# Kernel optimization log

Hardware: AMD Instinct MI355X
Metric: run time of the kernel (lower is better)

Reference implementation:

```python
import jax, jax.numpy as jnp
import numpy as np

DN = ('NCHW', 'OIHW', 'NCHW')

def _conv(x, w, b=None):
    # x: [P, C, H, W], w: [1, C, k, k] -> [P, 1, H, W] with SAME padding
    y = jax.lax.conv_general_dilated(x, w, (1, 1), 'SAME', dimension_numbers=DN)
    if b is not None:
        y = y + b[None, :, None, None]
    return y

def setup_inputs() -> dict:
    key = jax.random.key(0)
    ks = jax.random.split(key, 6)
    T, P, H, W = 36, 64, 128, 256
    K = 5
    inputs = jax.random.normal(ks[0], (T, P, H, W), dtype=jnp.float32)
    w_reset = 0.1 * jax.random.normal(ks[1], (1, 2, K, K), dtype=jnp.float32)
    b_reset = jnp.zeros((1,), dtype=jnp.float32)
    w_update = 0.1 * jax.random.normal(ks[2], (1, 2, K, K), dtype=jnp.float32)
    b_update = jnp.zeros((1,), dtype=jnp.float32)
    w_out = 0.1 * jax.random.normal(ks[3], (1, 2, K, K), dtype=jnp.float32)
    gam = jnp.ones((P,), dtype=jnp.float32)
    add_weights = 0.02 * jax.random.normal(ks[4], (P, H, W), dtype=jnp.float32)
    bias = jnp.zeros((H, W), dtype=jnp.float32)
    return {"inputs": inputs, "w_reset": w_reset, "b_reset": b_reset,
            "w_update": w_update, "b_update": b_update, "w_out": w_out,
            "gam": gam, "add_weights": add_weights, "bias": bias}

def reference(inputs, w_reset, b_reset, w_update, b_update, w_out, gam, add_weights, bias):
    # inputs: [T, P, H, W]; renormalize by per-plant scale gam
    x = gam[None, :, None, None] * inputs
    x = x[:, :, None]  # [T, P, 1, H, W] (channel dim = 1)
    h0 = jnp.zeros_like(x[0])  # [P, 1, H, W]

    def step(h, xt):
        stacked = jnp.concatenate([xt, h], axis=1)  # [P, 2, H, W]
        u = jax.nn.sigmoid(_conv(stacked, w_update, b_update))  # update gate
        r = jax.nn.sigmoid(_conv(stacked, w_reset, b_reset))    # reset gate
        c = _conv(jnp.concatenate([xt, r * h], axis=1), w_out)  # candidate (no bias, no act)
        h_new = h * (1.0 - u) + c * u
        return h_new, h_new

    _, states = jax.lax.scan(step, h0, x)  # [T, P, 1, H, W]
    s = states[:, :, 0]  # [T, P, H, W]
    # final layer (additive=False, rnn_act=None): tanh then per-plant spatial weights
    xs = jnp.tanh(s) * add_weights[None]
    out_y = xs.sum(axis=1) + bias[None]  # [T, H, W]
    return out_y, xs
```

## Files before the change

kernel.cpp:

```cpp
#include <hip/hip_runtime.h>

constexpr int T = 36, P = 64, H = 128, W = 256;
constexpr int HW  = H * W;
constexpr int PHW = P * HW;

constexpr int TH   = 16;
constexpr int NB   = 8;
constexpr int NBLK = P * NB;
constexpr int SR = 25, SC = 268;
constexpr int RR = 20;

constexpr long long TMO_ARRIVE = 3000000;
constexpr long long TMO_STEP   = 1000000;

typedef float vfloat4 __attribute__((ext_vector_type(4)));

__device__ __forceinline__ float fast_sigmoid(float z) {
    float e = __expf(-z);
    return __builtin_amdgcn_rcpf(1.0f + e);
}
__device__ __forceinline__ float fast_tanh(float x) {
    float e = __expf(-2.0f * fabsf(x));
    float t = (1.0f - e) * __builtin_amdgcn_rcpf(1.0f + e);
    return copysignf(t, x);
}

__device__ __forceinline__ void lds_store4(float* d, float4 v) {
    *(float2*)d       = make_float2(v.x, v.y);
    *(float2*)(d + 2) = make_float2(v.z, v.w);
}

__global__ __launch_bounds__(512, 4) void gru_all(
    const float* __restrict__ inputs, const float* __restrict__ gam,
    const float* __restrict__ w_update, const float* __restrict__ b_update,
    const float* __restrict__ w_reset,  const float* __restrict__ b_reset,
    const float* __restrict__ w_out,    const float* __restrict__ add_w,
    float* __restrict__ xs, float* __restrict__ hhalo, int* __restrict__ flags)
{
    __shared__ __align__(16) float sx[SR][SC];
    __shared__ __align__(16) float sh[SR][SC];
    __shared__ __align__(16) float srh[RR][SC];
    __shared__ int s_nowait;

    const int tid  = threadIdx.x;
    const int bid  = blockIdx.x;
    const int p    = bid >> 3;
    const int band = bid & 7;
    const int y0   = band * TH;

    const float gamma = gam[p];
    const float bu = b_update[0];
    const float br = b_reset[0];

    const int cg = tid & 63, rbb = tid >> 6;
    const int ox = 4 * cg,   oy  = 2 * rbb;

    int* flagsTop = flags;
    int* flagsBot = flags + NBLK;

    if (tid == 0) {
        s_nowait = 0;
        __hip_atomic_fetch_add(&flags[2 * NBLK], 1, __ATOMIC_RELAXED, __HIP_MEMORY_SCOPE_AGENT);
        const long long t0 = (long long)__builtin_amdgcn_s_memrealtime();
        while (__hip_atomic_load(&flags[2 * NBLK], __ATOMIC_RELAXED, __HIP_MEMORY_SCOPE_AGENT) < NBLK) {
            __builtin_amdgcn_s_sleep(16);
            if ((long long)__builtin_amdgcn_s_memrealtime() - t0 > TMO_ARRIVE) { s_nowait = 1; break; }
        }
    }

    float4 aw4[2];
    #pragma unroll
    for (int k = 0; k < 2; ++k)
        aw4[k] = *(const float4*)&add_w[(size_t)p * HW + (y0 + oy + k) * W + ox];

    for (int s = tid; s < SR * SC; s += 512) {
        (&sx[0][0])[s] = 0.f;
        (&sh[0][0])[s] = 0.f;
    }
    __syncthreads();
    {
        const float* xt = inputs + (size_t)p * HW;
        #pragma unroll
        for (int k = 0; k < 3; ++k) {
            const int s = tid + 512 * k;
            const int r = s >> 6, c4 = s & 63;
            const int gy = y0 + r - 4;
            if ((unsigned)gy < (unsigned)H) {
                float4 v = *(const float4*)&xt[gy * W + 4 * c4];
                v.x *= gamma; v.y *= gamma; v.z *= gamma; v.w *= gamma;
                lds_store4(&sx[r][6 + 4 * c4], v);
            }
        }
    }
    __syncthreads();

    float4 hn4_prev[2];

    #pragma unroll 1
    for (int t = 0; t < T; ++t) {
        if (t > 0) {
            float* xso = xs + (size_t)(t - 1) * PHW + (size_t)p * HW;
            #pragma unroll
            for (int k = 0; k < 2; ++k) {
                vfloat4 v;
                v.x = fast_tanh(hn4_prev[k].x) * aw4[k].x;
                v.y = fast_tanh(hn4_prev[k].y) * aw4[k].y;
                v.z = fast_tanh(hn4_prev[k].z) * aw4[k].z;
                v.w = fast_tanh(hn4_prev[k].w) * aw4[k].w;
                __builtin_nontemporal_store(v, (vfloat4*)&xso[(y0 + oy + k) * W + ox]);
            }
        }

        if (tid < 462) {
            const int b  = tid / 66;
            const int g  = tid - 66 * b;
            const int r0 = 3 * b;
            const int c0 = 4 * g;
            float racc[3][4], hold[3][4];
            #pragma unroll
            for (int k = 0; k < 3; ++k)
                #pragma unroll
                for (int c = 0; c < 4; ++c) racc[k][c] = br;
            #pragma unroll
            for (int ir = 0; ir < 7; ++ir) {
                const float4 xa = *(const float4*)&sx[r0 + ir][c0];
                const float4 xb = *(const float4*)&sx[r0 + ir][c0 + 4];
                const float4 ha = *(const float4*)&sh[r0 + ir][c0];
                const float4 hb = *(const float4*)&sh[r0 + ir][c0 + 4];
                const float vx[8] = {xa.x, xa.y, xa.z, xa.w, xb.x, xb.y, xb.z, xb.w};
                const float vh[8] = {ha.x, ha.y, ha.z, ha.w, hb.x, hb.y, hb.z, hb.w};
                if (ir >= 2 && ir <= 4) {
                    #pragma unroll
                    for (int c = 0; c < 4; ++c) hold[ir - 2][c] = vh[c + 2];
                }
                #pragma unroll
                for (int k = 0; k < 3; ++k) {
                    const int dy = ir - k;
                    if (dy >= 0 && dy <= 4) {
                        #pragma unroll
                        for (int dx = 0; dx < 5; ++dx) {
                            const float wx = w_reset[dy * 5 + dx];
                            const float wh = w_reset[25 + dy * 5 + dx];
                            #pragma unroll
                            for (int c = 0; c < 4; ++c) {
                                racc[k][c] = fmaf(vx[c + dx], wx, racc[k][c]);
                                racc[k][c] = fmaf(vh[c + dx], wh, racc[k][c]);
                            }
                        }
                    }
                }
            }
            #pragma unroll
            for (int k = 0; k < 3; ++k) {
                if (r0 + k < RR) {
                    float4 v;
                    v.x = fast_sigmoid(racc[k][0]) * hold[k][0];
                    v.y = fast_sigmoid(racc[k][1]) * hold[k][1];
                    v.z = fast_sigmoid(racc[k][2]) * hold[k][2];
                    v.w = fast_sigmoid(racc[k][3]) * hold[k][3];
                    lds_store4(&srh[r0 + k][c0 + 2], v);
                }
            }
        }
        __syncthreads();

        float4 hn4[2];
        {
            float uacc[2][4], cacc[2][4], hold[2][4];
            #pragma unroll
            for (int k = 0; k < 2; ++k)
                #pragma unroll
                for (int c = 0; c < 4; ++c) { uacc[k][c] = bu; cacc[k][c] = 0.f; }
            #pragma unroll
            for (int ir = 0; ir < 6; ++ir) {
                const int sr = oy + 2 + ir;
                const float4 xa = *(const float4*)&sx[sr][ox + 4];
                const float4 xb = *(const float4*)&sx[sr][ox + 8];
                const float4 ha = *(const float4*)&sh[sr][ox + 4];
                const float4 hb = *(const float4*)&sh[sr][ox + 8];
                const float4 ra = *(const float4*)&srh[oy + ir][ox + 4];
                const float4 rb = *(const float4*)&srh[oy + ir][ox + 8];
                const float vx[8] = {xa.x, xa.y, xa.z, xa.w, xb.x, xb.y, xb.z, xb.w};
                const float vh[8] = {ha.x, ha.y, ha.z, ha.w, hb.x, hb.y, hb.z, hb.w};
                const float vr[8] = {ra.x, ra.y, ra.z, ra.w, rb.x, rb.y, rb.z, rb.w};
                if (ir == 2) {
                    #pragma unroll
                    for (int c = 0; c < 4; ++c) hold[0][c] = vh[c + 2];
                }
                if (ir == 3) {
                    #pragma unroll
                    for (int c = 0; c < 4; ++c) hold[1][c] = vh[c + 2];
                }
                #pragma unroll
                for (int k = 0; k < 2; ++k) {
                    const int dy = ir - k;
                    if (dy >= 0 && dy <= 4) {
                        #pragma unroll
                        for (int dx = 0; dx < 5; ++dx) {
                            const float wux = w_update[dy * 5 + dx];
                            const float wuh = w_update[25 + dy * 5 + dx];
                            const float wox = w_out[dy * 5 + dx];
                            const float wor = w_out[25 + dy * 5 + dx];
                            #pragma unroll
                            for (int c = 0; c < 4; ++c) {
                                uacc[k][c] = fmaf(vx[c + dx], wux, uacc[k][c]);
                                uacc[k][c] = fmaf(vh[c + dx], wuh, uacc[k][c]);
                                cacc[k][c] = fmaf(vx[c + dx], wox, cacc[k][c]);
                                cacc[k][c] = fmaf(vr[c + dx], wor, cacc[k][c]);
                            }
                        }
                    }
                }
            }
            #pragma unroll
            for (int k = 0; k < 2; ++k) {
                float hn[4];
                #pragma unroll
                for (int c = 0; c < 4; ++c) {
                    const float u = fast_sigmoid(uacc[k][c]);
                    hn[c] = hold[k][c] + (cacc[k][c] - hold[k][c]) * u;
                }
                hn4[k] = make_float4(hn[0], hn[1], hn[2], hn[3]);
            }
        }
        __syncthreads();

        if (t + 1 < T) {
            if (rbb < 2 && band > 0) {
                float* hb = hhalo + (size_t)(t & 1) * (NBLK * 2048) + (size_t)bid * 2048;
                #pragma unroll
                for (int k = 0; k < 2; ++k) {
                    float* d = &hb[(oy + k) * 256 + ox];
                    __hip_atomic_store(&d[0], hn4[k].x, __ATOMIC_RELAXED, __HIP_MEMORY_SCOPE_AGENT);
                    __hip_atomic_store(&d[1], hn4[k].y, __ATOMIC_RELAXED, __HIP_MEMORY_SCOPE_AGENT);
                    __hip_atomic_store(&d[2], hn4[k].z, __ATOMIC_RELAXED, __HIP_MEMORY_SCOPE_AGENT);
                    __hip_atomic_store(&d[3], hn4[k].w, __ATOMIC_RELAXED, __HIP_MEMORY_SCOPE_AGENT);
                }
                asm volatile("s_waitcnt vmcnt(0)" ::: "memory");
                if (cg == 0)
                    __hip_atomic_fetch_add(&flagsTop[bid], 1, __ATOMIC_RELAXED, __HIP_MEMORY_SCOPE_AGENT);
            }
            if (rbb >= 6 && band < 7) {
                float* hb = hhalo + (size_t)(t & 1) * (NBLK * 2048) + (size_t)bid * 2048;
                #pragma unroll
                for (int k = 0; k < 2; ++k) {
                    float* d = &hb[(oy + k - 8) * 256 + ox];
                    __hip_atomic_store(&d[0], hn4[k].x, __ATOMIC_RELAXED, __HIP_MEMORY_SCOPE_AGENT);
                    __hip_atomic_store(&d[1], hn4[k].y, __ATOMIC_RELAXED, __HIP_MEMORY_SCOPE_AGENT);
                    __hip_atomic_store(&d[2], hn4[k].z, __ATOMIC_RELAXED, __HIP_MEMORY_SCOPE_AGENT);
                    __hip_atomic_store(&d[3], hn4[k].w, __ATOMIC_RELAXED, __HIP_MEMORY_SCOPE_AGENT);
                }
                asm volatile("s_waitcnt vmcnt(0)" ::: "memory");
                if (cg == 0)
                    __hip_atomic_fetch_add(&flagsBot[bid], 1, __ATOMIC_RELAXED, __HIP_MEMORY_SCOPE_AGENT);
            }
        }

        #pragma unroll
        for (int k = 0; k < 2; ++k)
            lds_store4(&sh[4 + oy + k][6 + ox], hn4[k]);
        if (t + 1 < T) {
            const float* xt = inputs + (size_t)(t + 1) * PHW + (size_t)p * HW;
            #pragma unroll
            for (int k = 0; k < 3; ++k) {
                const int s = tid + 512 * k;
                const int r = s >> 6, c4 = s & 63;
                const int gy = y0 + r - 4;
                if ((unsigned)gy < (unsigned)H) {
                    float4 v = *(const float4*)&xt[gy * W + 4 * c4];
                    v.x *= gamma; v.y *= gamma; v.z *= gamma; v.w *= gamma;
                    lds_store4(&sx[r][6 + 4 * c4], v);
                }
            }
        }

        hn4_prev[0] = hn4[0];
        hn4_prev[1] = hn4[1];
        if (t + 1 >= T) break;

        if (tid == 0 && band > 0 && !s_nowait) {
            const long long t0 = (long long)__builtin_amdgcn_s_memrealtime();
            while (__hip_atomic_load(&flagsBot[bid - 1], __ATOMIC_RELAXED, __HIP_MEMORY_SCOPE_AGENT) < 2 * (t + 1)) {
                __builtin_amdgcn_s_sleep(1);
                if ((long long)__builtin_amdgcn_s_memrealtime() - t0 > TMO_STEP) { s_nowait = 1; break; }
            }
        }
        if (tid == 64 && band < 7 && !s_nowait) {
            const long long t0 = (long long)__builtin_amdgcn_s_memrealtime();
            while (__hip_atomic_load(&flagsTop[bid + 1], __ATOMIC_RELAXED, __HIP_MEMORY_SCOPE_AGENT) < 2 * (t + 1)) {
                __builtin_amdgcn_s_sleep(1);
                if ((long long)__builtin_amdgcn_s_memrealtime() - t0 > TMO_STEP) { s_nowait = 1; break; }
            }
        }
        __syncthreads();

        {
            float* hb0 = hhalo + (size_t)(t & 1) * (NBLK * 2048);
            const int r = tid >> 6, c4 = tid & 63;
            if (r < 4) {
                if (band > 0) {
                    float* src = &hb0[(size_t)(bid - 1) * 2048 + (4 + r) * 256 + 4 * c4];
                    float4 v;
                    v.x = __hip_atomic_load(&src[0], __ATOMIC_RELAXED, __HIP_MEMORY_SCOPE_AGENT);
                    v.y = __hip_atomic_load(&src[1], __ATOMIC_RELAXED, __HIP_MEMORY_SCOPE_AGENT);
                    v.z = __hip_atomic_load(&src[2], __ATOMIC_RELAXED, __HIP_MEMORY_SCOPE_AGENT);
                    v.w = __hip_atomic_load(&src[3], __ATOMIC_RELAXED, __HIP_MEMORY_SCOPE_AGENT);
                    lds_store4(&sh[r][6 + 4 * c4], v);
                }
            } else {
                if (band < 7) {
                    float* src = &hb0[(size_t)(bid + 1) * 2048 + (r - 4) * 256 + 4 * c4];
                    float4 v;
                    v.x = __hip_atomic_load(&src[0], __ATOMIC_RELAXED, __HIP_MEMORY_SCOPE_AGENT);
                    v.y = __hip_atomic_load(&src[1], __ATOMIC_RELAXED, __HIP_MEMORY_SCOPE_AGENT);
                    v.z = __hip_atomic_load(&src[2], __ATOMIC_RELAXED, __HIP_MEMORY_SCOPE_AGENT);
                    v.w = __hip_atomic_load(&src[3], __ATOMIC_RELAXED, __HIP_MEMORY_SCOPE_AGENT);
                    lds_store4(&sh[16 + r][6 + 4 * c4], v);
                }
            }
        }
        __syncthreads();
    }

    {
        float* xso = xs + (size_t)(T - 1) * PHW + (size_t)p * HW;
        #pragma unroll
        for (int k = 0; k < 2; ++k) {
            vfloat4 v;
            v.x = fast_tanh(hn4_prev[k].x) * aw4[k].x;
            v.y = fast_tanh(hn4_prev[k].y) * aw4[k].y;
            v.z = fast_tanh(hn4_prev[k].z) * aw4[k].z;
            v.w = fast_tanh(hn4_prev[k].w) * aw4[k].w;
            __builtin_nontemporal_store(v, (vfloat4*)&xso[(y0 + oy + k) * W + ox]);
        }
    }
}

__global__ __launch_bounds__(256) void reduce_out(
    const float* __restrict__ xs, const float* __restrict__ bias,
    float* __restrict__ out_y)
{
    const int i4  = blockIdx.x * 256 + threadIdx.x;
    const int t   = i4 / (HW / 4);
    const int yx4 = i4 - t * (HW / 4);
    const float4* __restrict__ src = (const float4*)(xs + (size_t)t * PHW) + yx4;
    const float4  b4 = ((const float4*)bias)[yx4];
    float a0[4] = {b4.x, b4.y, b4.z, b4.w};
    float a1[4] = {0.f, 0.f, 0.f, 0.f};
    #pragma unroll 8
    for (int p = 0; p < P; p += 2) {
        const float4 v0 = src[(size_t)p * (HW / 4)];
        const float4 v1 = src[(size_t)(p + 1) * (HW / 4)];
        a0[0] += v0.x; a0[1] += v0.y; a0[2] += v0.z; a0[3] += v0.w;
        a1[0] += v1.x; a1[1] += v1.y; a1[2] += v1.z; a1[3] += v1.w;
    }
    ((float4*)out_y)[i4] = make_float4(a0[0] + a1[0], a0[1] + a1[1],
                                       a0[2] + a1[2], a0[3] + a1[3]);
}

extern "C" void kernel_launch(void* const* d_in, const int* in_sizes, int n_in,
                              void* d_out, int out_size, void* d_ws, size_t ws_size,
                              hipStream_t stream) {
    const float* inputs   = (const float*)d_in[0];
    const float* w_reset  = (const float*)d_in[1];
    const float* b_reset  = (const float*)d_in[2];
    const float* w_update = (const float*)d_in[3];
    const float* b_update = (const float*)d_in[4];
    const float* w_out    = (const float*)d_in[5];
    const float* gam      = (const float*)d_in[6];
    const float* add_w    = (const float*)d_in[7];
    const float* bias     = (const float*)d_in[8];

    float* out_y = (float*)d_out;
    float* xs    = out_y + (size_t)T * HW;

    float* hhalo = (float*)d_ws;
    int*   flags = (int*)((char*)d_ws + (size_t)2 * NBLK * 2048 * sizeof(float));

    (void)hipMemsetAsync(flags, 0, (2 * NBLK + 1) * sizeof(int), stream);

    gru_all<<<dim3(NBLK), dim3(512), 0, stream>>>(
        inputs, gam, w_update, b_update, w_reset, b_reset, w_out, add_w,
        xs, hhalo, flags);

    const int nout4 = T * HW / 4;
    reduce_out<<<nout4 / 256, 256, 0, stream>>>(xs, bias, out_y);
}
```

Before: 761.8 us.

## Load inputs directly to LDS, fold gamma into conv, remap blocks and phase-1 work

Input tiles are now copied straight from global memory into LDS with global_load_lds, skipping the register round trip. The gamma scale is no longer applied at load time; it is folded into the gate and candidate accumulators through separate x and h accumulators. Block indexing changes to band-major (p = bid & 63), and phase-1 reset-gate work is remapped so each full wave owns one row band, which avoids divide-by-66 indexing and partial waves. The split accumulators add registers and the extra fma, and the neighbour-band flag and halo indices move to bid±64.

Measured after the change: 829.7 us. 1.09x slower.

```diff
diff --git a/kernel.cpp b/kernel.cpp
--- a/kernel.cpp
+++ b/kernel.cpp
@@ -1,4 +1,5 @@
 #include <hip/hip_runtime.h>
+#include <stdint.h>
 
 constexpr int T = 36, P = 64, H = 128, W = 256;
 constexpr int HW  = H * W;
@@ -14,6 +15,8 @@
 constexpr long long TMO_STEP   = 1000000;
 
 typedef float vfloat4 __attribute__((ext_vector_type(4)));
+#define GLB_AS __attribute__((address_space(1)))
+#define LDS_AS __attribute__((address_space(3)))
 
 __device__ __forceinline__ float fast_sigmoid(float z) {
     float e = __expf(-z);
@@ -44,16 +47,16 @@
 
     const int tid  = threadIdx.x;
     const int bid  = blockIdx.x;
-    const int p    = bid >> 3;
-    const int band = bid & 7;
+    const int p    = bid & 63;
+    const int band = bid >> 6;
     const int y0   = band * TH;
 
     const float gamma = gam[p];
     const float bu = b_update[0];
     const float br = b_reset[0];
 
-    const int cg = tid & 63, rbb = tid >> 6;
-    const int ox = 4 * cg,   oy  = 2 * rbb;
+    const int lane = tid & 63, rbb = tid >> 6;
+    const int ox = 4 * lane, oy = 2 * rbb;
 
     int* flagsTop = flags;
     int* flagsBot = flags + NBLK;
@@ -82,17 +85,66 @@
         const float* xt = inputs + (size_t)p * HW;
         #pragma unroll
         for (int k = 0; k < 3; ++k) {
-            const int s = tid + 512 * k;
-            const int r = s >> 6, c4 = s & 63;
+            const int r  = rbb + 8 * k;
             const int gy = y0 + r - 4;
             if ((unsigned)gy < (unsigned)H) {
-                float4 v = *(const float4*)&xt[gy * W + 4 * c4];
-                v.x *= gamma; v.y *= gamma; v.z *= gamma; v.w *= gamma;
-                lds_store4(&sx[r][6 + 4 * c4], v);
+                __builtin_amdgcn_global_load_lds(
+                    (const GLB_AS uint32_t*)(xt + gy * W + 4 * lane),
+                    (LDS_AS uint32_t*)&sx[r][6], 16, 0, 0);
             }
         }
     }
     __syncthreads();
+
+    auto ph1_slot = [&](int b, int g) {
+        const int r0 = 3 * b;
+        const int c0 = 4 * g;
+        float rx[3][4], rh[3][4], hold[3][4];
+        #pragma unroll
+        for (int k = 0; k < 3; ++k)
+            #pragma unroll
+            for (int c = 0; c < 4; ++c) { rx[k][c] = 0.f; rh[k][c] = br; }
+        #pragma unroll
+        for (int ir = 0; ir < 7; ++ir) {
+            const float4 xa = *(const float4*)&sx[r0 + ir][c0];
+            const float4 xb = *(const float4*)&sx[r0 + ir][c0 + 4];
+            const float4 ha = *(const float4*)&sh[r0 + ir][c0];
+            const float4 hb = *(const float4*)&sh[r0 + ir][c0 + 4];
+            const float vx[8] = {xa.x, xa.y, xa.z, xa.w, xb.x, xb.y, xb.z, xb.w};
+            const float vh[8] = {ha.x, ha.y, ha.z, ha.w, hb.x, hb.y, hb.z, hb.w};
+            if (ir >= 2 && ir <= 4) {
+                #pragma unroll
+                for (int c = 0; c < 4; ++c) hold[ir - 2][c] = vh[c + 2];
+            }
+            #pragma unroll
+            for (int k = 0; k < 3; ++k) {
+                const int dy = ir - k;
+                if (dy >= 0 && dy <= 4) {
+                    #pragma unroll
+                    for (int dx = 0; dx < 5; ++dx) {
+                        const float wx = w_reset[dy * 5 + dx];
+                        const float wh = w_reset[25 + dy * 5 + dx];
+                        #pragma unroll
+                        for (int c = 0; c < 4; ++c) {
+                            rx[k][c] = fmaf(vx[c + dx], wx, rx[k][c]);
+                            rh[k][c] = fmaf(vh[c + dx], wh, rh[k][c]);
+                        }
+                    }
+                }
+            }
+        }
+        #pragma unroll
+        for (int k = 0; k < 3; ++k) {
+            if (r0 + k < RR) {
+                float4 v;
+                v.x = fast_sigmoid(fmaf(gamma, rx[k][0], rh[k][0])) * hold[k][0];
+                v.y = fast_sigmoid(fmaf(gamma, rx[k][1], rh[k][1])) * hold[k][1];
+                v.z = fast_sigmoid(fmaf(gamma, rx[k][2], rh[k][2])) * hold[k][2];
+                v.w = fast_sigmoid(fmaf(gamma, rx[k][3], rh[k][3])) * hold[k][3];
+                lds_store4(&srh[r0 + k][c0 + 2], v);
+            }
+        }
+    };
 
     float4 hn4_prev[2];
 
@@ -111,66 +163,19 @@
             }
         }
 
-        if (tid < 462) {
-            const int b  = tid / 66;
-            const int g  = tid - 66 * b;
-            const int r0 = 3 * b;
-            const int c0 = 4 * g;
-            float racc[3][4], hold[3][4];
-            #pragma unroll
-            for (int k = 0; k < 3; ++k)
-                #pragma unroll
-                for (int c = 0; c < 4; ++c) racc[k][c] = br;
-            #pragma unroll
-            for (int ir = 0; ir < 7; ++ir) {
-                const float4 xa = *(const float4*)&sx[r0 + ir][c0];
-                const float4 xb = *(const float4*)&sx[r0 + ir][c0 + 4];
-                const float4 ha = *(const float4*)&sh[r0 + ir][c0];
-                const float4 hb = *(const float4*)&sh[r0 + ir][c0 + 4];
-                const float vx[8] = {xa.x, xa.y, xa.z, xa.w, xb.x, xb.y, xb.z, xb.w};
-                const float vh[8] = {ha.x, ha.y, ha.z, ha.w, hb.x, hb.y, hb.z, hb.w};
-                if (ir >= 2 && ir <= 4) {
-                    #pragma unroll
-                    for (int c = 0; c < 4; ++c) hold[ir - 2][c] = vh[c + 2];
-                }
-                #pragma unroll
-                for (int k = 0; k < 3; ++k) {
-                    const int dy = ir - k;
-                    if (dy >= 0 && dy <= 4) {
-                        #pragma unroll
-                        for (int dx = 0; dx < 5; ++dx) {
-                            const float wx = w_reset[dy * 5 + dx];
-                            const float wh = w_reset[25 + dy * 5 + dx];
-                            #pragma unroll
-                            for (int c = 0; c < 4; ++c) {
-                                racc[k][c] = fmaf(vx[c + dx], wx, racc[k][c]);
-                                racc[k][c] = fmaf(vh[c + dx], wh, racc[k][c]);
-                            }
-                        }
-                    }
-                }
-            }
-            #pragma unroll
-            for (int k = 0; k < 3; ++k) {
-                if (r0 + k < RR) {
-                    float4 v;
-                    v.x = fast_sigmoid(racc[k][0]) * hold[k][0];
-                    v.y = fast_sigmoid(racc[k][1]) * hold[k][1];
-                    v.z = fast_sigmoid(racc[k][2]) * hold[k][2];
-                    v.w = fast_sigmoid(racc[k][3]) * hold[k][3];
-                    lds_store4(&srh[r0 + k][c0 + 2], v);
-                }
-            }
-        }
+        if (rbb < 7)          ph1_slot(rbb, lane);
+        else if (lane < 14)   ph1_slot(lane >> 1, 64 + (lane & 1));
         __syncthreads();
 
         float4 hn4[2];
         {
-            float uacc[2][4], cacc[2][4], hold[2][4];
+            float ux[2][4], uh[2][4], cx[2][4], crh[2][4], hold[2][4];
             #pragma unroll
             for (int k = 0; k < 2; ++k)
                 #pragma unroll
-                for (int c = 0; c < 4; ++c) { uacc[k][c] = bu; cacc[k][c] = 0.f; }
+                for (int c = 0; c < 4; ++c) {
+                    ux[k][c] = 0.f; uh[k][c] = bu; cx[k][c] = 0.f; crh[k][c] = 0.f;
+                }
             #pragma unroll
             for (int ir = 0; ir < 6; ++ir) {
                 const int sr = oy + 2 + ir;
@@ -203,10 +208,10 @@
                             const float wor = w_out[25 + dy * 5 + dx];
                             #pragma unroll
                             for (int c = 0; c < 4; ++c) {
-                                uacc[k][c] = fmaf(vx[c + dx], wux, uacc[k][c]);
-                                uacc[k][c] = fmaf(vh[c + dx], wuh, uacc[k][c]);
-                                cacc[k][c] = fmaf(vx[c + dx], wox, cacc[k][c]);
-                                cacc[k][c] = fmaf(vr[c + dx], wor, cacc[k][c]);
+                                ux[k][c]  = fmaf(vx[c + dx], wux, ux[k][c]);
+                                uh[k][c]  = fmaf(vh[c + dx], wuh, uh[k][c]);
+                                cx[k][c]  = fmaf(vx[c + dx], wox, cx[k][c]);
+                                crh[k][c] = fmaf(vr[c + dx], wor, crh[k][c]);
                             }
                         }
                     }
@@ -217,8 +222,9 @@
                 float hn[4];
                 #pragma unroll
                 for (int c = 0; c < 4; ++c) {
-                    const float u = fast_sigmoid(uacc[k][c]);
-                    hn[c] = hold[k][c] + (cacc[k][c] - hold[k][c]) * u;
+                    const float u  = fast_sigmoid(fmaf(gamma, ux[k][c], uh[k][c]));
+                    const float cc = fmaf(gamma, cx[k][c], crh[k][c]);
+                    hn[c] = hold[k][c] + (cc - hold[k][c]) * u;
                 }
                 hn4[k] = make_float4(hn[0], hn[1], hn[2], hn[3]);
             }
@@ -237,7 +243,7 @@
                     __hip_atomic_store(&d[3], hn4[k].w, __ATOMIC_RELAXED, __HIP_MEMORY_SCOPE_AGENT);
                 }
                 asm volatile("s_waitcnt vmcnt(0)" ::: "memory");
-                if (cg == 0)
+                if (lane == 0)
                     __hip_atomic_fetch_add(&flagsTop[bid], 1, __ATOMIC_RELAXED, __HIP_MEMORY_SCOPE_AGENT);
             }
             if (rbb >= 6 && band < 7) {
@@ -251,7 +257,7 @@
                     __hip_atomic_store(&d[3], hn4[k].w, __ATOMIC_RELAXED, __HIP_MEMORY_SCOPE_AGENT);
                 }
                 asm volatile("s_waitcnt vmcnt(0)" ::: "memory");
-                if (cg == 0)
+                if (lane == 0)
                     __hip_atomic_fetch_add(&flagsBot[bid], 1, __ATOMIC_RELAXED, __HIP_MEMORY_SCOPE_AGENT);
             }
         }
@@ -263,13 +269,12 @@
             const float* xt = inputs + (size_t)(t + 1) * PHW + (size_t)p * HW;
             #pragma unroll
             for (int k = 0; k < 3; ++k) {
-                const int s = tid + 512 * k;
-                const int r = s >> 6, c4 = s & 63;
+                const int r  = rbb + 8 * k;
                 const int gy = y0 + r - 4;
                 if ((unsigned)gy < (unsigned)H) {
-                    float4 v = *(const float4*)&xt[gy * W + 4 * c4];
-                    v.x *= gamma; v.y *= gamma; v.z *= gamma; v.w *= gamma;
-                    lds_store4(&sx[r][6 + 4 * c4], v);
+                    __builtin_amdgcn_global_load_lds(
+                        (const GLB_AS uint32_t*)(xt + gy * W + 4 * lane),
+                        (LDS_AS uint32_t*)&sx[r][6], 16, 0, 0);
                 }
             }
         }
@@ -280,14 +285,14 @@
 
         if (tid == 0 && band > 0 && !s_nowait) {
             const long long t0 = (long long)__builtin_amdgcn_s_memrealtime();
-            while (__hip_atomic_load(&flagsBot[bid - 1], __ATOMIC_RELAXED, __HIP_MEMORY_SCOPE_AGENT) < 2 * (t + 1)) {
+            while (__hip_atomic_load(&flagsBot[bid - 64], __ATOMIC_RELAXED, __HIP_MEMORY_SCOPE_AGENT) < 2 * (t + 1)) {
                 __builtin_amdgcn_s_sleep(1);
                 if ((long long)__builtin_amdgcn_s_memrealtime() - t0 > TMO_STEP) { s_nowait = 1; break; }
             }
         }
         if (tid == 64 && band < 7 && !s_nowait) {
             const long long t0 = (long long)__builtin_amdgcn_s_memrealtime();
-            while (__hip_atomic_load(&flagsTop[bid + 1], __ATOMIC_RELAXED, __HIP_MEMORY_SCOPE_AGENT) < 2 * (t + 1)) {
+            while (__hip_atomic_load(&flagsTop[bid + 64], __ATOMIC_RELAXED, __HIP_MEMORY_SCOPE_AGENT) < 2 * (t + 1)) {
                 __builtin_amdgcn_s_sleep(1);
                 if ((long long)__builtin_amdgcn_s_memrealtime() - t0 > TMO_STEP) { s_nowait = 1; break; }
             }
@@ -299,7 +304,7 @@
             const int r = tid >> 6, c4 = tid & 63;
             if (r < 4) {
                 if (band > 0) {
-                    float* src = &hb0[(size_t)(bid - 1) * 2048 + (4 + r) * 256 + 4 * c4];
+                    float* src = &hb0[(size_t)(bid - 64) * 2048 + (4 + r) * 256 + 4 * c4];
                     float4 v;
                     v.x = __hip_atomic_load(&src[0], __ATOMIC_RELAXED, __HIP_MEMORY_SCOPE_AGENT);
                     v.y = __hip_atomic_load(&src[1], __ATOMIC_RELAXED, __HIP_MEMORY_SCOPE_AGENT);
@@ -309,7 +314,7 @@
                 }
             } else {
                 if (band < 7) {
-                    float* src = &hb0[(size_t)(bid + 1) * 2048 + (r - 4) * 256 + 4 * c4];
+                    float* src = &hb0[(size_t)(bid + 64) * 2048 + (r - 4) * 256 + 4 * c4];
                     float4 v;
                     v.x = __hip_atomic_load(&src[0], __ATOMIC_RELAXED, __HIP_MEMORY_SCOPE_AGENT);
                     v.y = __hip_atomic_load(&src[1], __ATOMIC_RELAXED, __HIP_MEMORY_SCOPE_AGENT);
```
